# Optimization experiments

Measured on AMD Instinct MI355X. Metric: run time of the kernel, lower is better.

Reference implementation:

```python
import jax, jax.numpy as jnp
from jax import lax
import numpy as np

KSIZE = 3
NUM_GAB = 16
NUM_IMAP = 16
BATCH = 4096


def gabor_bank(theta, sigma, gamma, lambd, psi, ksize=KSIZE):
    # vectorized version of the original triple Python loop
    offs = jnp.arange(ksize, dtype=theta.dtype) - 1.0  # (x-1), (y-1) in source
    xg, yg = jnp.meshgrid(offs, offs, indexing='ij')   # [K,K]
    c = jnp.cos(theta)[:, None, None]
    s = jnp.sin(theta)[:, None, None]
    xt = xg * c + yg * s        # [F,K,K]
    yt = -xg * s + yg * c
    sx = sigma[:, None, None]
    sy = (sigma / gamma)[:, None, None]
    env = jnp.exp(-0.5 * (xt ** 2 / sx ** 2 + yt ** 2 / sy ** 2))
    car = jnp.cos(2.0 * jnp.pi * xt / lambd[:, None, None] + psi[:, None, None])
    return env * car  # [F,K,K]


def maxpool2(x):
    return lax.reduce_window(x, -jnp.inf, lax.max, (1, 1, 2, 2), (1, 1, 2, 2), 'VALID')


def setup_inputs() -> dict:
    key = jax.random.key(0)
    ks = jax.random.split(key, 12)
    x = jax.random.normal(ks[0], (BATCH, 1, 28, 28), dtype=jnp.float32)
    theta = jax.random.uniform(ks[1], (NUM_GAB,), minval=0.0, maxval=180.0)
    sigma = jax.random.uniform(ks[2], (NUM_GAB,), minval=0.0, maxval=360.0)
    gamma = jax.random.uniform(ks[3], (NUM_GAB,), minval=0.0, maxval=1.0)
    lambd = jax.random.uniform(ks[4], (NUM_GAB,), minval=2.0, maxval=10.0)
    psi = jnp.zeros((NUM_GAB,), dtype=jnp.float32)
    conv2_w = jax.random.normal(ks[5], (64, 32, 3, 3), dtype=jnp.float32) * 0.05
    conv2_b = jnp.zeros((64,), dtype=jnp.float32)
    fc1_w = jax.random.normal(ks[6], (128, 3136), dtype=jnp.float32) * 0.02
    fc1_b = jnp.zeros((128,), dtype=jnp.float32)
    fc2_w = jax.random.normal(ks[7], (10, 128), dtype=jnp.float32) * 0.1
    fc2_b = jnp.zeros((10,), dtype=jnp.float32)
    return dict(x=x, theta=theta, sigma=sigma, gamma=gamma, lambd=lambd, psi=psi,
                conv2_w=conv2_w, conv2_b=conv2_b, fc1_w=fc1_w, fc1_b=fc1_b,
                fc2_w=fc2_w, fc2_b=fc2_b)


def reference(x, theta, sigma, gamma, lambd, psi, conv2_w, conv2_b, fc1_w, fc1_b, fc2_w, fc2_b):
    kern = gabor_bank(theta, sigma, gamma, lambd, psi)          # [16,3,3]
    imaps = jnp.zeros((NUM_IMAP, KSIZE, KSIZE), dtype=x.dtype).at[:, 1, 1].set(1.0)
    w1 = jnp.concatenate([kern, imaps], axis=0)[:, None]         # [32,1,3,3]
    dn = ('NCHW', 'OIHW', 'NCHW')
    out = lax.conv_general_dilated(x, w1, (1, 1), [(1, 1), (1, 1)], dimension_numbers=dn)
    out = maxpool2(jax.nn.relu(out))                             # [B,32,14,14]
    out = lax.conv_general_dilated(out, conv2_w, (1, 1), [(1, 1), (1, 1)], dimension_numbers=dn)
    out = maxpool2(jax.nn.relu(out + conv2_b[None, :, None, None]))  # [B,64,7,7]
    out = out.reshape(out.shape[0], -1)                          # [B,3136]
    out = jax.nn.relu(out @ fc1_w.T + fc1_b)                     # dropout = identity (eval)
    out = out @ fc2_w.T + fc2_b                                  # [B,10]
    return out
```

## Files before the change

kernel.cpp:

```cpp
#include <hip/hip_runtime.h>
#include <hip/hip_bf16.h>

#define BATCH 4096

typedef unsigned short u16;
typedef _Float16 half2v __attribute__((ext_vector_type(2)));
typedef _Float16 half4 __attribute__((ext_vector_type(4)));
typedef _Float16 half8 __attribute__((ext_vector_type(8)));
typedef short bs8 __attribute__((ext_vector_type(8)));
typedef u16 u16x4 __attribute__((ext_vector_type(4)));
typedef float floatx4 __attribute__((ext_vector_type(4)));
typedef float floatx16 __attribute__((ext_vector_type(16)));

__device__ inline u16 f2bf_hw(float f) {
    __hip_bfloat16 b = __float2bfloat16(f);
    return *(u16*)&b;
}

__global__ __launch_bounds__(256) void prep_kernel(
        const float* __restrict__ theta, const float* __restrict__ sigma,
        const float* __restrict__ gamma, const float* __restrict__ lambd,
        const float* __restrict__ psi, const float* __restrict__ conv2_w,
        const float* __restrict__ fc1_w, _Float16* __restrict__ w1h,
        _Float16* __restrict__ w2h, u16* __restrict__ wbf) {
    int id = blockIdx.x * 256 + threadIdx.x;
    if (id < 512) {
        int g = id >> 4, t = id & 15;
        float v = 0.0f;
        if (t < 9) {
            int i = t / 3, j = t % 3;
            float xg = (float)i - 1.0f;
            float yg = (float)j - 1.0f;
            if (g < 16) {
                float th = theta[g];
                float c = cosf(th), s = sinf(th);
                float xt = xg * c + yg * s;
                float yt = -xg * s + yg * c;
                float sx = sigma[g];
                float sy = sx / gamma[g];
                float env = expf(-0.5f *
                                 (xt * xt / (sx * sx) + yt * yt / (sy * sy)));
                float car =
                    cosf(6.28318530717958647692f * xt / lambd[g] + psi[g]);
                v = env * car;
            } else {
                v = (t == 4) ? 1.0f : 0.0f;
            }
        }
        w1h[id] = (_Float16)v;
    } else if (id < 512 + 18432) {
        int t2 = id - 512;
        int tap = t2 / 2048, rem = t2 % 2048;
        int oc = rem / 32, k = rem % 32;
        int ic = (k >> 1) + 16 * (k & 1);
        w2h[t2] = (_Float16)conv2_w[(oc * 32 + ic) * 9 + tap];
    } else {
        int i4 = id - 18944;
        int s = i4 >> 10;
        int q = i4 & 1023;
        int row = q >> 3;
        int kp = s * 32 + (q & 7) * 4;
        int pl = kp >> 6;
        int ocb = kp & 63;
        const float* src = fc1_w + row * 3136 + ocb * 49 + pl;
        u16x4 o;
        o[0] = f2bf_hw(src[0]);
        o[1] = f2bf_hw(src[49]);
        o[2] = f2bf_hw(src[98]);
        o[3] = f2bf_hw(src[147]);
        ((u16x4*)wbf)[(size_t)s * 1024 + row * 8 + (q & 7)] = o;
    }
}

__global__ __launch_bounds__(256, 4) void fused_conv_kernel(
        const float* __restrict__ x, const _Float16* __restrict__ w1h,
        const _Float16* __restrict__ w2h, const float* __restrict__ conv2_b,
        u16* __restrict__ a2) {
    __shared__ _Float16 img16[30][36];
    __shared__ __align__(16) _Float16 a1s[16][16][40];
    __shared__ __align__(16) u16 out2[64 * 49];

    int t = threadIdx.x;
    int n = blockIdx.x;
    int lane = t & 63;
    int w = t >> 6;
    int l16 = lane & 15;
    int quad = lane >> 4;
    int l32 = lane & 31;
    int h = lane >> 5;

    int nt = w & 1;
    int mt0 = w >> 1;
    int oc = nt * 32 + l32;

    for (int i = t; i < 240; i += 256) {
        int pos = i >> 2, ch = i & 3;
        int r, c;
        if (pos < 16)      { r = 0;        c = pos; }
        else if (pos < 32) { r = 15;       c = pos - 16; }
        else if (pos < 46) { r = pos - 31; c = 0; }
        else               { r = pos - 45; c = 15; }
        *(int4*)&a1s[r][c][ch * 8] = int4{0, 0, 0, 0};
    }
    const float* xim = x + (size_t)n * 784;
    for (int i = t; i < 960; i += 256) {
        int r = i >> 5, c = i & 31;
        bool inter = (r >= 1) & (r <= 28) & (c >= 1) & (c <= 28);
        float v = inter ? xim[(r - 1) * 28 + (c - 1)] : 0.0f;
        img16[r][c] = (_Float16)v;
    }
    __syncthreads();

    half4 b1a = *(const half4*)&w1h[l16 * 16 + quad * 4];
    half4 b1b = *(const half4*)&w1h[(16 + l16) * 16 + quad * 4];
    int t0 = quad * 4;
    int u0 = t0 < 9 ? t0 : 8, u1 = t0 + 1 < 9 ? t0 + 1 : 8;
    int u2 = t0 + 2 < 9 ? t0 + 2 : 8, u3 = t0 + 3 < 9 ? t0 + 3 : 8;
    int off0 = (u0 / 3) * 36 + (u0 % 3);
    int off1 = (u1 / 3) * 36 + (u1 % 3);
    int off2 = (u2 / 3) * 36 + (u2 % 3);
    int off3 = (u3 / 3) * 36 + (u3 % 3);
    int sy = (l16 & 3) >> 1, sx = l16 & 1;

    int pool0 = w * 4 + (l16 >> 2);
    int a14 = pool0 >= 14 ? 1 : 0;
    int b14 = pool0 - 14 * a14;
    int pl0 = w * 4 + quad;
    int pa = pl0 >= 14 ? 1 : 0;
    int pb = pl0 - 14 * pa;

    for (int mt = w; mt < 49; mt += 4) {
        const _Float16* p = &img16[2 * a14 + sy][2 * b14 + sx];
        half4 av;
        av[0] = p[off0];
        av[1] = p[off1];
        av[2] = p[off2];
        av[3] = p[off3];
        floatx4 c0 = {0.f, 0.f, 0.f, 0.f};
        floatx4 c1 = {0.f, 0.f, 0.f, 0.f};
        c0 = __builtin_amdgcn_mfma_f32_16x16x16f16(av, b1a, c0, 0, 0, 0);
        c1 = __builtin_amdgcn_mfma_f32_16x16x16f16(av, b1b, c1, 0, 0, 0);
        float m0 = fmaxf(fmaxf(c0[0], c0[1]), fmaxf(c0[2], c0[3]));
        float m1 = fmaxf(fmaxf(c1[0], c1[1]), fmaxf(c1[2], c1[3]));
        half2v pk;
        pk[0] = (_Float16)fmaxf(m0, 0.0f);
        pk[1] = (_Float16)fmaxf(m1, 0.0f);
        *(half2v*)&a1s[1 + pa][1 + pb][2 * l16] = pk;
        a14 += 1; b14 += 2;
        if (b14 >= 14) { b14 -= 14; a14 += 1; }
        pa += 1; pb += 2;
        if (pb >= 14) { pb -= 14; pa += 1; }
    }

    half8 bE[9], bO[9];
    const _Float16* bp = w2h + (size_t)oc * 32 + h * 8;
#pragma unroll
    for (int tt = 0; tt < 9; ++tt) {
        bE[tt] = *(const half8*)(bp + tt * 2048);
        bO[tt] = *(const half8*)(bp + tt * 2048 + 16);
    }
    float bias = conv2_b[oc];
    __syncthreads();

    for (int mt = mt0; mt < 7; mt += 2) {
        int pool = mt * 8 + (l32 >> 2);
        int sub = l32 & 3;
        int pc = pool < 49 ? pool : 48;
        int y = 2 * (pc / 7) + (sub >> 1);
        int xq = 2 * (pc % 7) + (sub & 1);
        const _Float16* ap = &a1s[y][xq][h * 8];
        floatx16 acc = {};
#pragma unroll
        for (int tt = 0; tt < 9; ++tt) {
            int ao = ((tt / 3) * 16 + (tt % 3)) * 40;
            half8 avE = *(const half8*)(ap + ao);
            half8 avO = *(const half8*)(ap + ao + 16);
            acc = __builtin_amdgcn_mfma_f32_32x32x16_f16(avE, bE[tt], acc,
                                                         0, 0, 0);
            acc = __builtin_amdgcn_mfma_f32_32x32x16_f16(avO, bO[tt], acc,
                                                         0, 0, 0);
        }
#pragma unroll
        for (int rg = 0; rg < 4; ++rg) {
            int pl = mt * 8 + 2 * rg + h;
            if (pl < 49) {
                float v0 = acc[rg * 4 + 0];
                float v1 = acc[rg * 4 + 1];
                float v2 = acc[rg * 4 + 2];
                float v3 = acc[rg * 4 + 3];
                float mx = fmaxf(fmaxf(v0, v1), fmaxf(v2, v3));
                out2[pl * 64 + oc] = f2bf_hw(fmaxf(mx + bias, 0.0f));
            }
        }
    }
    __syncthreads();

    uint2* dst = (uint2*)a2;
    const uint2* src = (const uint2*)&out2[0];
    size_t n8 = (size_t)n * 8;
    for (int i = t; i < 784; i += 256) {
        int s = i >> 3, off = i & 7;
        dst[(size_t)s * 32768 + n8 + off] = src[i];
    }
}

__global__ __launch_bounds__(1024) void fc_kernel(
        const u16* __restrict__ A, const u16* __restrict__ Wbf,
        const float* __restrict__ fc1_b, const float* __restrict__ fc2_w,
        const float* __restrict__ fc2_b, float* __restrict__ out) {
    __shared__ float Hs[8][16][132];
    int tid = threadIdx.x;
    int lane = tid & 63;
    int w = tid >> 6;
    int l16 = lane & 15;
    int quad = lane >> 4;
    int kq = w >> 1;
    int nh = w & 1;
    int m0 = blockIdx.x * 16;

    const u16* abase = A + (size_t)(m0 + l16) * 32 + quad * 8;
    const u16* bbase = Wbf + (size_t)(nh * 64 + l16) * 32 + quad * 8;

    floatx4 ac0 = {0.f, 0.f, 0.f, 0.f};
    floatx4 ac1 = {0.f, 0.f, 0.f, 0.f};
    floatx4 ac2 = {0.f, 0.f, 0.f, 0.f};
    floatx4 ac3 = {0.f, 0.f, 0.f, 0.f};
#pragma unroll 4
    for (int s = kq; s < 98; s += 8) {
        bs8 av = *(const bs8*)(abase + (size_t)s * 131072);
        const u16* bt = bbase + (size_t)s * 4096;
        bs8 bv0 = *(const bs8*)(bt);
        bs8 bv1 = *(const bs8*)(bt + 512);
        bs8 bv2 = *(const bs8*)(bt + 1024);
        bs8 bv3 = *(const bs8*)(bt + 1536);
        ac0 = __builtin_amdgcn_mfma_f32_16x16x32_bf16(av, bv0, ac0, 0, 0, 0);
        ac1 = __builtin_amdgcn_mfma_f32_16x16x32_bf16(av, bv1, ac1, 0, 0, 0);
        ac2 = __builtin_amdgcn_mfma_f32_16x16x32_bf16(av, bv2, ac2, 0, 0, 0);
        ac3 = __builtin_amdgcn_mfma_f32_16x16x32_bf16(av, bv3, ac3, 0, 0, 0);
    }
    int nb = nh * 64 + l16;
#pragma unroll
    for (int r = 0; r < 4; ++r) {
        int mr = quad * 4 + r;
        Hs[kq][mr][nb] = ac0[r];
        Hs[kq][mr][nb + 16] = ac1[r];
        Hs[kq][mr][nb + 32] = ac2[r];
        Hs[kq][mr][nb + 48] = ac3[r];
    }
    __syncthreads();

    for (int i = tid; i < 2048; i += 1024) {
        int m = i >> 7, k = i & 127;
        float s = Hs[0][m][k] + Hs[1][m][k] + Hs[2][m][k] + Hs[3][m][k] +
                  Hs[4][m][k] + Hs[5][m][k] + Hs[6][m][k] + Hs[7][m][k];
        Hs[0][m][k] = s;
    }
    __syncthreads();

    if (tid < 160) {
        int m = tid / 10, j = tid % 10;
        const float* wr = fc2_w + j * 128;
        float acc = fc2_b[j];
#pragma unroll 16
        for (int k = 0; k < 128; ++k)
            acc += fmaxf(Hs[0][m][k] + fc1_b[k], 0.0f) * wr[k];
        out[(size_t)(m0 + m) * 10 + j] = acc;
    }
}

extern "C" void kernel_launch(void* const* d_in, const int* in_sizes, int n_in,
                              void* d_out, int out_size, void* d_ws,
                              size_t ws_size, hipStream_t stream) {
    const float* x       = (const float*)d_in[0];
    const float* theta   = (const float*)d_in[1];
    const float* sigma   = (const float*)d_in[2];
    const float* gamma   = (const float*)d_in[3];
    const float* lambd   = (const float*)d_in[4];
    const float* psi     = (const float*)d_in[5];
    const float* conv2_w = (const float*)d_in[6];
    const float* conv2_b = (const float*)d_in[7];
    const float* fc1_w   = (const float*)d_in[8];
    const float* fc1_b   = (const float*)d_in[9];
    const float* fc2_w   = (const float*)d_in[10];
    const float* fc2_b   = (const float*)d_in[11];
    float* out = (float*)d_out;

    char* ws = (char*)d_ws;
    u16* a2 = (u16*)ws;
    _Float16* w1h = (_Float16*)(ws + 25690112ull);
    _Float16* w2h = (_Float16*)(ws + 25691136ull);
    u16* wbf = (u16*)(ws + 25728000ull);

    prep_kernel<<<466, 256, 0, stream>>>(theta, sigma, gamma, lambd, psi,
                                         conv2_w, fc1_w, w1h, w2h, wbf);
    fused_conv_kernel<<<BATCH, 256, 0, stream>>>(x, w1h, w2h, conv2_b, a2);
    fc_kernel<<<BATCH / 16, 1024, 0, stream>>>(a2, wbf, fc1_b, fc2_w, fc2_b,
                                               out);
}
```

Before: 148.8 us.

## Process two images per conv block and prefetch the second image during conv1

```diff
diff --git a/kernel.cpp b/kernel.cpp
--- a/kernel.cpp
+++ b/kernel.cpp
@@ -81,7 +81,7 @@
     __shared__ __align__(16) u16 out2[64 * 49];
 
     int t = threadIdx.x;
-    int n = blockIdx.x;
+    int n0 = blockIdx.x * 2;
     int lane = t & 63;
     int w = t >> 6;
     int l16 = lane & 15;
@@ -92,24 +92,6 @@
     int nt = w & 1;
     int mt0 = w >> 1;
     int oc = nt * 32 + l32;
-
-    for (int i = t; i < 240; i += 256) {
-        int pos = i >> 2, ch = i & 3;
-        int r, c;
-        if (pos < 16)      { r = 0;        c = pos; }
-        else if (pos < 32) { r = 15;       c = pos - 16; }
-        else if (pos < 46) { r = pos - 31; c = 0; }
-        else               { r = pos - 45; c = 15; }
-        *(int4*)&a1s[r][c][ch * 8] = int4{0, 0, 0, 0};
-    }
-    const float* xim = x + (size_t)n * 784;
-    for (int i = t; i < 960; i += 256) {
-        int r = i >> 5, c = i & 31;
-        bool inter = (r >= 1) & (r <= 28) & (c >= 1) & (c <= 28);
-        float v = inter ? xim[(r - 1) * 28 + (c - 1)] : 0.0f;
-        img16[r][c] = (_Float16)v;
-    }
-    __syncthreads();
 
     half4 b1a = *(const half4*)&w1h[l16 * 16 + quad * 4];
     half4 b1b = *(const half4*)&w1h[(16 + l16) * 16 + quad * 4];
@@ -123,85 +105,136 @@
     int sy = (l16 & 3) >> 1, sx = l16 & 1;
 
     int pool0 = w * 4 + (l16 >> 2);
-    int a14 = pool0 >= 14 ? 1 : 0;
-    int b14 = pool0 - 14 * a14;
+    int a14_s = pool0 >= 14 ? 1 : 0;
+    int b14_s = pool0 - 14 * a14_s;
     int pl0 = w * 4 + quad;
-    int pa = pl0 >= 14 ? 1 : 0;
-    int pb = pl0 - 14 * pa;
-
-    for (int mt = w; mt < 49; mt += 4) {
-        const _Float16* p = &img16[2 * a14 + sy][2 * b14 + sx];
-        half4 av;
-        av[0] = p[off0];
-        av[1] = p[off1];
-        av[2] = p[off2];
-        av[3] = p[off3];
-        floatx4 c0 = {0.f, 0.f, 0.f, 0.f};
-        floatx4 c1 = {0.f, 0.f, 0.f, 0.f};
-        c0 = __builtin_amdgcn_mfma_f32_16x16x16f16(av, b1a, c0, 0, 0, 0);
-        c1 = __builtin_amdgcn_mfma_f32_16x16x16f16(av, b1b, c1, 0, 0, 0);
-        float m0 = fmaxf(fmaxf(c0[0], c0[1]), fmaxf(c0[2], c0[3]));
-        float m1 = fmaxf(fmaxf(c1[0], c1[1]), fmaxf(c1[2], c1[3]));
-        half2v pk;
-        pk[0] = (_Float16)fmaxf(m0, 0.0f);
-        pk[1] = (_Float16)fmaxf(m1, 0.0f);
-        *(half2v*)&a1s[1 + pa][1 + pb][2 * l16] = pk;
-        a14 += 1; b14 += 2;
-        if (b14 >= 14) { b14 -= 14; a14 += 1; }
-        pa += 1; pb += 2;
-        if (pb >= 14) { pb -= 14; pa += 1; }
-    }
-
+    int pa_s = pl0 >= 14 ? 1 : 0;
+    int pb_s = pl0 - 14 * pa_s;
+
+    auto conv1_body = [&]() {
+        int a14 = a14_s, b14 = b14_s, pa = pa_s, pb = pb_s;
+        for (int mt = w; mt < 49; mt += 4) {
+            const _Float16* p = &img16[2 * a14 + sy][2 * b14 + sx];
+            half4 av;
+            av[0] = p[off0];
+            av[1] = p[off1];
+            av[2] = p[off2];
+            av[3] = p[off3];
+            floatx4 c0 = {0.f, 0.f, 0.f, 0.f};
+            floatx4 c1 = {0.f, 0.f, 0.f, 0.f};
+            c0 = __builtin_amdgcn_mfma_f32_16x16x16f16(av, b1a, c0, 0, 0, 0);
+            c1 = __builtin_amdgcn_mfma_f32_16x16x16f16(av, b1b, c1, 0, 0, 0);
+            float m0 = fmaxf(fmaxf(c0[0], c0[1]), fmaxf(c0[2], c0[3]));
+            float m1 = fmaxf(fmaxf(c1[0], c1[1]), fmaxf(c1[2], c1[3]));
+            half2v pk;
+            pk[0] = (_Float16)fmaxf(m0, 0.0f);
+            pk[1] = (_Float16)fmaxf(m1, 0.0f);
+            *(half2v*)&a1s[1 + pa][1 + pb][2 * l16] = pk;
+            a14 += 1; b14 += 2;
+            if (b14 >= 14) { b14 -= 14; a14 += 1; }
+            pa += 1; pb += 2;
+            if (pb >= 14) { pb -= 14; pa += 1; }
+        }
+    };
+
+    if (t < 240) {
+        int pos = t >> 2, ch = t & 3;
+        int r, c;
+        if (pos < 16)      { r = 0;        c = pos; }
+        else if (pos < 32) { r = 15;       c = pos - 16; }
+        else if (pos < 46) { r = pos - 31; c = 0; }
+        else               { r = pos - 45; c = 15; }
+        *(int4*)&a1s[r][c][ch * 8] = int4{0, 0, 0, 0};
+    }
+    const float* xim0 = x + (size_t)n0 * 784;
+    for (int i = t; i < 960; i += 256) {
+        int r = i >> 5, c = i & 31;
+        bool inter = (r >= 1) & (r <= 28) & (c >= 1) & (c <= 28);
+        float v = inter ? xim0[(r - 1) * 28 + (c - 1)] : 0.0f;
+        img16[r][c] = (_Float16)v;
+    }
+    __syncthreads();
+
+    const float* xim1 = x + (size_t)(n0 + 1) * 784;
+    float gx[4];
+#pragma unroll
+    for (int j = 0; j < 4; ++j) {
+        int i = t + j * 256;
+        gx[j] = (i < 784) ? xim1[i] : 0.0f;
+    }
+    conv1_body();
     half8 bE[9], bO[9];
-    const _Float16* bp = w2h + (size_t)oc * 32 + h * 8;
-#pragma unroll
-    for (int tt = 0; tt < 9; ++tt) {
-        bE[tt] = *(const half8*)(bp + tt * 2048);
-        bO[tt] = *(const half8*)(bp + tt * 2048 + 16);
+    {
+        const _Float16* bp = w2h + (size_t)oc * 32 + h * 8;
+#pragma unroll
+        for (int tt = 0; tt < 9; ++tt) {
+            bE[tt] = *(const half8*)(bp + tt * 2048);
+            bO[tt] = *(const half8*)(bp + tt * 2048 + 16);
+        }
     }
     float bias = conv2_b[oc];
     __syncthreads();
 
-    for (int mt = mt0; mt < 7; mt += 2) {
-        int pool = mt * 8 + (l32 >> 2);
-        int sub = l32 & 3;
-        int pc = pool < 49 ? pool : 48;
-        int y = 2 * (pc / 7) + (sub >> 1);
-        int xq = 2 * (pc % 7) + (sub & 1);
-        const _Float16* ap = &a1s[y][xq][h * 8];
-        floatx16 acc = {};
-#pragma unroll
-        for (int tt = 0; tt < 9; ++tt) {
-            int ao = ((tt / 3) * 16 + (tt % 3)) * 40;
-            half8 avE = *(const half8*)(ap + ao);
-            half8 avO = *(const half8*)(ap + ao + 16);
-            acc = __builtin_amdgcn_mfma_f32_32x32x16_f16(avE, bE[tt], acc,
-                                                         0, 0, 0);
-            acc = __builtin_amdgcn_mfma_f32_32x32x16_f16(avO, bO[tt], acc,
-                                                         0, 0, 0);
-        }
-#pragma unroll
-        for (int rg = 0; rg < 4; ++rg) {
-            int pl = mt * 8 + 2 * rg + h;
-            if (pl < 49) {
-                float v0 = acc[rg * 4 + 0];
-                float v1 = acc[rg * 4 + 1];
-                float v2 = acc[rg * 4 + 2];
-                float v3 = acc[rg * 4 + 3];
-                float mx = fmaxf(fmaxf(v0, v1), fmaxf(v2, v3));
-                out2[pl * 64 + oc] = f2bf_hw(fmaxf(mx + bias, 0.0f));
+    auto conv2_body = [&]() {
+        for (int mt = mt0; mt < 7; mt += 2) {
+            int pool = mt * 8 + (l32 >> 2);
+            int sub = l32 & 3;
+            int pc = pool < 49 ? pool : 48;
+            int y = 2 * (pc / 7) + (sub >> 1);
+            int xq = 2 * (pc % 7) + (sub & 1);
+            const _Float16* ap = &a1s[y][xq][h * 8];
+            floatx16 acc = {};
+#pragma unroll
+            for (int tt = 0; tt < 9; ++tt) {
+                int ao = ((tt / 3) * 16 + (tt % 3)) * 40;
+                half8 avE = *(const half8*)(ap + ao);
+                half8 avO = *(const half8*)(ap + ao + 16);
+                acc = __builtin_amdgcn_mfma_f32_32x32x16_f16(avE, bE[tt], acc,
+                                                             0, 0, 0);
+                acc = __builtin_amdgcn_mfma_f32_32x32x16_f16(avO, bO[tt], acc,
+                                                             0, 0, 0);
             }
-        }
-    }
-    __syncthreads();
-
-    uint2* dst = (uint2*)a2;
-    const uint2* src = (const uint2*)&out2[0];
-    size_t n8 = (size_t)n * 8;
-    for (int i = t; i < 784; i += 256) {
-        int s = i >> 3, off = i & 7;
-        dst[(size_t)s * 32768 + n8 + off] = src[i];
-    }
+#pragma unroll
+            for (int rg = 0; rg < 4; ++rg) {
+                int pl = mt * 8 + 2 * rg + h;
+                if (pl < 49) {
+                    float v0 = acc[rg * 4 + 0];
+                    float v1 = acc[rg * 4 + 1];
+                    float v2 = acc[rg * 4 + 2];
+                    float v3 = acc[rg * 4 + 3];
+                    float mx = fmaxf(fmaxf(v0, v1), fmaxf(v2, v3));
+                    out2[pl * 64 + oc] = f2bf_hw(fmaxf(mx + bias, 0.0f));
+                }
+            }
+        }
+    };
+
+    auto copyout = [&](int n) {
+        uint2* dst = (uint2*)a2;
+        const uint2* src = (const uint2*)&out2[0];
+        size_t n8 = (size_t)n * 8;
+        for (int i = t; i < 784; i += 256) {
+            int s = i >> 3, off = i & 7;
+            dst[(size_t)s * 32768 + n8 + off] = src[i];
+        }
+    };
+
+#pragma unroll
+    for (int j = 0; j < 4; ++j) {
+        int i = t + j * 256;
+        if (i < 784) img16[i / 28 + 1][i % 28 + 1] = (_Float16)gx[j];
+    }
+    conv2_body();
+    __syncthreads();
+
+    copyout(n0);
+    conv1_body();
+    __syncthreads();
+
+    conv2_body();
+    __syncthreads();
+
+    copyout(n0 + 1);
 }
 
 __global__ __launch_bounds__(1024) void fc_kernel(
@@ -293,7 +326,8 @@
 
     prep_kernel<<<466, 256, 0, stream>>>(theta, sigma, gamma, lambd, psi,
                                          conv2_w, fc1_w, w1h, w2h, wbf);
-    fused_conv_kernel<<<BATCH, 256, 0, stream>>>(x, w1h, w2h, conv2_b, a2);
+    fused_conv_kernel<<<BATCH / 2, 256, 0, stream>>>(x, w1h, w2h, conv2_b,
+                                                     a2);
     fc_kernel<<<BATCH / 16, 1024, 0, stream>>>(a2, wbf, fc1_b, fc2_w, fc2_b,
                                                out);
 }
```

Result: no change. 147.2 us, median of 2 (-1.0%).
